# Optimization experiments

Measured on AMD Instinct MI355X. Metric: run time of the kernel, lower is better.

The kernel has to match this reference:

```python
import jax, jax.numpy as jnp
import numpy as np

D_MODEL = 1024
B, S = 4, 4096


def setup_inputs() -> dict:
    key = jax.random.key(0)
    k1, k2, k3, k4, k5 = jax.random.split(key, 5)
    lim = 1.0 / np.sqrt(D_MODEL)  # nn.Linear default init range
    x = jax.random.normal(k1, (B, S, D_MODEL), dtype=jnp.float32)
    mask = jnp.ones((B, S), dtype=jnp.float32)
    W_up = jax.random.uniform(k2, (D_MODEL, D_MODEL), jnp.float32, -lim, lim)
    b_up = jax.random.uniform(k3, (D_MODEL,), jnp.float32, -lim, lim)
    W_f = jax.random.uniform(k4, (D_MODEL, D_MODEL), jnp.float32, -lim, lim)
    b_f = jax.random.uniform(k5, (D_MODEL,), jnp.float32, -lim, lim)
    decay_param = jnp.zeros((1,), dtype=jnp.float32)
    return {"x": x, "mask": mask, "W_up": W_up, "b_up": b_up,
            "W_f": W_f, "b_f": b_f, "decay_param": decay_param}


def _decay_scan(u, decay):
    # h_t = decay * h_{t-1} + u_t  along axis=1, via associative scan.
    # Element: (a, b) representing h -> a*h + b; compose: (a1*a2, b1*a2 + b2).
    a = jnp.broadcast_to(decay, u.shape)

    def combine(c1, c2):
        a1, b1 = c1
        a2, b2 = c2
        return a1 * a2, b1 * a2 + b2

    _, h = jax.lax.associative_scan(combine, (a, u), axis=1)
    return h


def reference(x, mask, W_up, b_up, W_f, b_f, decay_param):
    decay = jax.nn.sigmoid(decay_param)[0]
    # u_i = mask_i * linear_update(x_i)
    u = (jnp.einsum('bsd,ed->bse', x, W_up) + b_up) * mask[..., None]
    # h_t = sum_{i<=t} decay^(t-i) * u_i  (exponential-decay recurrence)
    h = _decay_scan(u, decay)
    return jnp.einsum('bsd,ed->bse', h, W_f) + b_f
```

## Files before the change

### kernel.cpp

```cpp
#include <hip/hip_runtime.h>
#include <hip/hip_bf16.h>
#include <cstdint>
#include <cstddef>

#define DMODEL 1024
#define BATCH  4
#define SEQ    4096
#define BSROWS (BATCH*SEQ)
#define CHUNK  32
#define NCHUNK (SEQ/CHUNK)

typedef __attribute__((ext_vector_type(8))) short bf16x8;
typedef __attribute__((ext_vector_type(4))) float f32x4;


__device__ __forceinline__ unsigned short f2bf(float f) {
  union { float f; uint32_t u; } v; v.f = f;
  uint32_t u = v.u;
  u += 0x7FFFu + ((u >> 16) & 1u);
  return (unsigned short)(u >> 16);
}

__device__ __forceinline__ float sigmoid_dev(const float* dp) {
  return 1.0f / (1.0f + expf(-dp[0]));
}

typedef __attribute__((address_space(1))) void void_g;
typedef __attribute__((address_space(3))) void void_l;

__device__ __forceinline__ void gl2lds16(const void* g, void* l) {
  __builtin_amdgcn_global_load_lds((void_g*)g, (void_l*)l, 16, 0, 0);
}

__global__ __launch_bounds__(256) void prep_kernel(
    const float* __restrict__ x, const float* __restrict__ mask,
    const float* __restrict__ W_up, const float* __restrict__ b_up,
    const float* __restrict__ W_f, const float* __restrict__ dp,
    unsigned short* __restrict__ Wf_bf, unsigned short* __restrict__ WupT,
    float* __restrict__ bb, float* __restrict__ carry,
    float* __restrict__ cbeta) {
  __shared__ float tile[32][33];
  int blk = blockIdx.x;
  int tid = threadIdx.x;

  if (blk < 512) {
    float decay = sigmoid_dev(dp);
    int b = blk / NCHUNK, c = blk % NCHUNK;
    const float4* xp = (const float4*)(x + ((size_t)(b * SEQ + c * CHUNK)) * DMODEL);
    const float* mp = mask + b * SEQ + c * CHUNK;
    float4 h = make_float4(0.f, 0.f, 0.f, 0.f);
    float hb = 0.f;
    #pragma unroll 8
    for (int s = 0; s < CHUNK; ++s) {
      float m = mp[s];
      float4 xv = xp[(size_t)s * (DMODEL / 4) + tid];
      h.x = decay * h.x + m * xv.x;
      h.y = decay * h.y + m * xv.y;
      h.z = decay * h.z + m * xv.z;
      h.w = decay * h.w + m * xv.w;
      hb = decay * hb + m;
    }
    ((float4*)carry)[(size_t)blk * (DMODEL / 4) + tid] = h;
    if (tid == 0) cbeta[blk] = hb;
  } else if (blk < 1536) {
    int i = (blk - 512) * 256 + tid;
    float4 v = ((const float4*)W_f)[i];
    ushort4 o;
    o.x = f2bf(v.x); o.y = f2bf(v.y); o.z = f2bf(v.z); o.w = f2bf(v.w);
    ((ushort4*)Wf_bf)[i] = o;
  } else if (blk < 2560) {
    int id = blk - 1536;
    int bx = id & 31, by = id >> 5;
    int tx = tid & 31, ty = tid >> 5;
    int xx = bx * 32 + tx;
    int y0 = by * 32;
    for (int j = ty; j < 32; j += 8)
      tile[j][tx] = W_up[(size_t)(y0 + j) * DMODEL + xx];
    __syncthreads();
    int ox = by * 32 + tx;
    int oy0 = bx * 32;
    for (int j = ty; j < 32; j += 8)
      WupT[(size_t)(oy0 + j) * DMODEL + ox] = f2bf(tile[tx][j]);
  } else {
    int w = tid >> 6;
    int lane = tid & 63;
    int e = (blk - 2560) * 4 + w;
    float s = 0.f;
    for (int i = lane; i < DMODEL; i += 64)
      s += W_f[(size_t)e * DMODEL + i] * b_up[i];
    #pragma unroll
    for (int off = 32; off; off >>= 1) s += __shfl_down(s, off);
    if (lane == 0) bb[e] = s;
  }
}

__global__ __launch_bounds__(64) void scan_chunk(
    const float* __restrict__ carry, const float* __restrict__ carry_beta,
    const float* __restrict__ dp, float* __restrict__ prefix,
    float* __restrict__ prefix_beta) {
  float decay = sigmoid_dev(dp);
  float dL = powf(decay, (float)CHUNK);
  int gid = blockIdx.x * 64 + threadIdx.x;
  int b = gid >> 10, d = gid & 1023;
  float P = 0.f;
  for (int c = 0; c < NCHUNK; c += 8) {
    float v[8];
    #pragma unroll
    for (int j = 0; j < 8; ++j)
      v[j] = carry[(size_t)(b * NCHUNK + c + j) * DMODEL + d];
    #pragma unroll
    for (int j = 0; j < 8; ++j) {
      prefix[(size_t)(b * NCHUNK + c + j) * DMODEL + d] = P;
      P = dL * P + v[j];
    }
  }
  if (d == 0) {
    float Pb = 0.f;
    for (int c = 0; c < NCHUNK; ++c) {
      prefix_beta[b * NCHUNK + c] = Pb;
      Pb = dL * Pb + carry_beta[b * NCHUNK + c];
    }
  }
}

__global__ __launch_bounds__(256) void mid_kernel(
    const unsigned short* __restrict__ A,
    const unsigned short* __restrict__ Bm,
    unsigned short* __restrict__ Wc,
    const float* __restrict__ x, const float* __restrict__ mask,
    const float* __restrict__ dp,
    const float* __restrict__ prefix, const float* __restrict__ prefix_beta,
    unsigned short* __restrict__ hv, float* __restrict__ hbeta) {
  __shared__ unsigned short As[64 * 32];
  __shared__ unsigned short Bs[64 * 32];
  int tid = threadIdx.x;
  if (blockIdx.x < 256) {
    int vb = blockIdx.x;
    int lane = tid & 63, w = tid >> 6;
    int wm = w & 1, wn = w >> 1;
    int m0 = (vb >> 4) * 64;
    int n0 = (vb & 15) * 64;
    int r = tid >> 2;
    int c8 = (tid & 3) * 8;
    f32x4 acc[2][2] = {};
    for (int k0 = 0; k0 < DMODEL; k0 += 32) {
      gl2lds16(A + (size_t)(m0 + r) * DMODEL + k0 + c8,  As + r * 32 + c8);
      gl2lds16(Bm + (size_t)(n0 + r) * DMODEL + k0 + c8, Bs + r * 32 + c8);
      __syncthreads();
      const bf16x8* Av = (const bf16x8*)As;
      const bf16x8* Bv = (const bf16x8*)Bs;
      int quad = lane >> 4, l16 = lane & 15;
      bf16x8 af[2], bfr[2];
      #pragma unroll
      for (int i = 0; i < 2; i++) {
        af[i]  = Av[(wm * 32 + i * 16 + l16) * 4 + quad];
        bfr[i] = Bv[(wn * 32 + i * 16 + l16) * 4 + quad];
      }
      #pragma unroll
      for (int i = 0; i < 2; i++)
        #pragma unroll
        for (int j = 0; j < 2; j++)
          acc[i][j] = __builtin_amdgcn_mfma_f32_16x16x32_bf16(af[i], bfr[j], acc[i][j], 0, 0, 0);
      __syncthreads();
    }
    int quad = lane >> 4, l16 = lane & 15;
    #pragma unroll
    for (int j = 0; j < 2; j++) {
      int col = n0 + wn * 32 + j * 16 + l16;
      #pragma unroll
      for (int i = 0; i < 2; i++) {
        int rowb = m0 + wm * 32 + i * 16 + quad * 4;
        #pragma unroll
        for (int rr = 0; rr < 4; ++rr)
          Wc[(size_t)(rowb + rr) * DMODEL + col] = f2bf(acc[i][j][rr]);
      }
    }
  } else {
    int vb = blockIdx.x - 256;
    float decay = sigmoid_dev(dp);
    int b = vb / NCHUNK, c = vb % NCHUNK;
    const float4* xp = (const float4*)(x + ((size_t)(b * SEQ + c * CHUNK)) * DMODEL);
    const float* mp = mask + b * SEQ + c * CHUNK;
    float4 h = ((const float4*)prefix)[(size_t)vb * (DMODEL / 4) + tid];
    float hb = prefix_beta[vb];
    #pragma unroll 8
    for (int s = 0; s < CHUNK; ++s) {
      float m = mp[s];
      float4 xv = xp[(size_t)s * (DMODEL / 4) + tid];
      h.x = decay * h.x + m * xv.x;
      h.y = decay * h.y + m * xv.y;
      h.z = decay * h.z + m * xv.z;
      h.w = decay * h.w + m * xv.w;
      hb = decay * hb + m;
      ushort4 o;
      o.x = f2bf(h.x); o.y = f2bf(h.y); o.z = f2bf(h.z); o.w = f2bf(h.w);
      int row = b * SEQ + c * CHUNK + s;
      ((ushort4*)hv)[(size_t)row * (DMODEL / 4) + tid] = o;
      if (tid == 0) hbeta[row] = hb;
    }
  }
}

__global__ __launch_bounds__(256) void gemm_main(
    const unsigned short* __restrict__ A,
    const unsigned short* __restrict__ Bm,
    const float* __restrict__ hbeta,
    const float* __restrict__ bb,
    const float* __restrict__ bias_f,
    float* __restrict__ out) {
  __shared__ unsigned short As[128 * 32];
  __shared__ unsigned short Bs[128 * 32];
  int tid = threadIdx.x;
  int lane = tid & 63, w = tid >> 6;
  int wm = w & 1, wn = w >> 1;
  int m0 = (blockIdx.x & 127) * 128;
  int n0 = (blockIdx.x >> 7) * 128;
  int r = tid >> 2;
  int c8 = (tid & 3) * 8;
  f32x4 acc[4][4] = {};
  for (int k0 = 0; k0 < DMODEL; k0 += 32) {
    gl2lds16(A + (size_t)(m0 + r) * DMODEL + k0 + c8,        As + r * 32 + c8);
    gl2lds16(A + (size_t)(m0 + 64 + r) * DMODEL + k0 + c8,   As + (64 + r) * 32 + c8);
    gl2lds16(Bm + (size_t)(n0 + r) * DMODEL + k0 + c8,       Bs + r * 32 + c8);
    gl2lds16(Bm + (size_t)(n0 + 64 + r) * DMODEL + k0 + c8,  Bs + (64 + r) * 32 + c8);
    __syncthreads();
    const bf16x8* Av = (const bf16x8*)As;
    const bf16x8* Bv = (const bf16x8*)Bs;
    int quad = lane >> 4, l16 = lane & 15;
    bf16x8 af[4], bfr[4];
    #pragma unroll
    for (int i = 0; i < 4; i++) {
      af[i]  = Av[(wm * 64 + i * 16 + l16) * 4 + quad];
      bfr[i] = Bv[(wn * 64 + i * 16 + l16) * 4 + quad];
    }
    #pragma unroll
    for (int i = 0; i < 4; i++)
      #pragma unroll
      for (int j = 0; j < 4; j++)
        acc[i][j] = __builtin_amdgcn_mfma_f32_16x16x32_bf16(af[i], bfr[j], acc[i][j], 0, 0, 0);
    __syncthreads();
  }
  int quad = lane >> 4, l16 = lane & 15;
  #pragma unroll
  for (int j = 0; j < 4; j++) {
    int col = n0 + wn * 64 + j * 16 + l16;
    float bbv = bb[col];
    float bfv = bias_f[col];
    #pragma unroll
    for (int i = 0; i < 4; i++) {
      int rowb = m0 + wm * 64 + i * 16 + quad * 4;
      #pragma unroll
      for (int rr = 0; rr < 4; ++rr) {
        int row = rowb + rr;
        out[(size_t)row * DMODEL + col] = acc[i][j][rr] + hbeta[row] * bbv + bfv;
      }
    }
  }
}


extern "C" void kernel_launch(void* const* d_in, const int* in_sizes, int n_in,
                              void* d_out, int out_size, void* d_ws, size_t ws_size,
                              hipStream_t stream) {
  const float* x    = (const float*)d_in[0];
  const float* mask = (const float*)d_in[1];
  const float* W_up = (const float*)d_in[2];
  const float* b_up = (const float*)d_in[3];
  const float* W_f  = (const float*)d_in[4];
  const float* b_f  = (const float*)d_in[5];
  const float* dp   = (const float*)d_in[6];
  float* out = (float*)d_out;

  char* ws = (char*)d_ws;
  unsigned short* hv    = (unsigned short*)(ws);
  unsigned short* Wc    = (unsigned short*)(ws + 33554432);
  unsigned short* Wf_bf = (unsigned short*)(ws + 35651584);
  unsigned short* WupT  = (unsigned short*)(ws + 37748736);
  float* carry  = (float*)(ws + 39845888);
  float* prefix = (float*)(ws + 41943040);
  float* hbeta  = (float*)(ws + 44040192);
  float* cbeta  = (float*)(ws + 44105728);
  float* pbeta  = (float*)(ws + 44107776);
  float* bb     = (float*)(ws + 44109824);

  prep_kernel<<<2816, 256, 0, stream>>>(x, mask, W_up, b_up, W_f, dp,
                                        Wf_bf, WupT, bb, carry, cbeta);
  scan_chunk<<<64, 64, 0, stream>>>(carry, cbeta, dp, prefix, pbeta);
  mid_kernel<<<768, 256, 0, stream>>>(Wf_bf, WupT, Wc, x, mask, dp,
                                      prefix, pbeta, hv, hbeta);
  gemm_main<<<1024, 256, 0, stream>>>(hv, Wc, hbeta, bb, b_f, out);
}
```

Measured before the change: 203.8 us.

## Decompose scan into local chunk scan plus projected chunk prefix correction

The prep kernel now writes the chunk-local scan of x (in bf16) directly, so the second full pass over x to apply chunk prefixes is gone. Cross-chunk prefixes are instead projected through the combined weight in a small GEMM (pout_kernel) and added in the main GEMM epilogue as decay^(s+1) times the projected prefix. The GEMMs also move to a K-step of 64 with an XOR-swizzled LDS layout to cut bank conflicts. In exchange there is an extra kernel launch and a small GEMM, plus an extra Pout read in the epilogue. Precision changes slightly because local scans are rounded to bf16 separately from the prefix term.

New measurement: 245.6 us. 1.21x slower.

```diff
diff --git a/kernel.cpp b/kernel.cpp
--- a/kernel.cpp
+++ b/kernel.cpp
@@ -9,6 +9,7 @@
 #define BSROWS (BATCH*SEQ)
 #define CHUNK  32
 #define NCHUNK (SEQ/CHUNK)
+#define NCH_T  (BATCH*NCHUNK)
 
 typedef __attribute__((ext_vector_type(8))) short bf16x8;
 typedef __attribute__((ext_vector_type(4))) float f32x4;
@@ -32,12 +33,49 @@
   __builtin_amdgcn_global_load_lds((void_g*)g, (void_l*)l, 16, 0, 0);
 }
 
+__device__ __forceinline__ void kloop64(
+    const unsigned short* __restrict__ A, const unsigned short* __restrict__ B,
+    int m0, int n0, f32x4 acc[2][2],
+    unsigned short* As, unsigned short* Bs, int tid) {
+  int lane = tid & 63, w = tid >> 6, wm = w & 1, wn = w >> 1;
+  int quad = lane >> 4, l16 = lane & 15;
+  int r = tid >> 3, cch = tid & 7;
+  int g = cch ^ (r & 7);
+  const bf16x8* Av = (const bf16x8*)As;
+  const bf16x8* Bv = (const bf16x8*)Bs;
+  for (int k0 = 0; k0 < DMODEL; k0 += 64) {
+    gl2lds16(A + (size_t)(m0 + r) * DMODEL + k0 + g * 8,      As + r * 64 + cch * 8);
+    gl2lds16(A + (size_t)(m0 + 32 + r) * DMODEL + k0 + g * 8, As + (32 + r) * 64 + cch * 8);
+    gl2lds16(B + (size_t)(n0 + r) * DMODEL + k0 + g * 8,      Bs + r * 64 + cch * 8);
+    gl2lds16(B + (size_t)(n0 + 32 + r) * DMODEL + k0 + g * 8, Bs + (32 + r) * 64 + cch * 8);
+    __syncthreads();
+    #pragma unroll
+    for (int kk = 0; kk < 2; ++kk) {
+      bf16x8 af[2], bfr[2];
+      #pragma unroll
+      for (int i = 0; i < 2; ++i) {
+        int rowA = wm * 32 + i * 16 + l16;
+        af[i]  = Av[rowA * 8 + ((kk * 4 + quad) ^ (l16 & 7))];
+        int rowB = wn * 32 + i * 16 + l16;
+        bfr[i] = Bv[rowB * 8 + ((kk * 4 + quad) ^ (l16 & 7))];
+      }
+      #pragma unroll
+      for (int i = 0; i < 2; ++i)
+        #pragma unroll
+        for (int j = 0; j < 2; ++j)
+          acc[i][j] = __builtin_amdgcn_mfma_f32_16x16x32_bf16(af[i], bfr[j], acc[i][j], 0, 0, 0);
+    }
+    __syncthreads();
+  }
+}
+
 __global__ __launch_bounds__(256) void prep_kernel(
     const float* __restrict__ x, const float* __restrict__ mask,
     const float* __restrict__ W_up, const float* __restrict__ b_up,
     const float* __restrict__ W_f, const float* __restrict__ dp,
     unsigned short* __restrict__ Wf_bf, unsigned short* __restrict__ WupT,
-    float* __restrict__ bb, float* __restrict__ carry,
+    float* __restrict__ bb, unsigned short* __restrict__ hv,
+    float* __restrict__ carry, float* __restrict__ lbeta,
     float* __restrict__ cbeta) {
   __shared__ float tile[32][33];
   int blk = blockIdx.x;
@@ -46,8 +84,9 @@
   if (blk < 512) {
     float decay = sigmoid_dev(dp);
     int b = blk / NCHUNK, c = blk % NCHUNK;
-    const float4* xp = (const float4*)(x + ((size_t)(b * SEQ + c * CHUNK)) * DMODEL);
-    const float* mp = mask + b * SEQ + c * CHUNK;
+    int base = b * SEQ + c * CHUNK;
+    const float4* xp = (const float4*)(x + (size_t)base * DMODEL);
+    const float* mp = mask + base;
     float4 h = make_float4(0.f, 0.f, 0.f, 0.f);
     float hb = 0.f;
     #pragma unroll 8
@@ -59,6 +98,10 @@
       h.z = decay * h.z + m * xv.z;
       h.w = decay * h.w + m * xv.w;
       hb = decay * hb + m;
+      ushort4 o;
+      o.x = f2bf(h.x); o.y = f2bf(h.y); o.z = f2bf(h.z); o.w = f2bf(h.w);
+      ((ushort4*)hv)[(size_t)(base + s) * (DMODEL / 4) + tid] = o;
+      if (tid == 0) lbeta[base + s] = hb;
     }
     ((float4*)carry)[(size_t)blk * (DMODEL / 4) + tid] = h;
     if (tid == 0) cbeta[blk] = hb;
@@ -94,109 +137,91 @@
   }
 }
 
-__global__ __launch_bounds__(64) void scan_chunk(
-    const float* __restrict__ carry, const float* __restrict__ carry_beta,
-    const float* __restrict__ dp, float* __restrict__ prefix,
-    float* __restrict__ prefix_beta) {
-  float decay = sigmoid_dev(dp);
-  float dL = powf(decay, (float)CHUNK);
-  int gid = blockIdx.x * 64 + threadIdx.x;
-  int b = gid >> 10, d = gid & 1023;
-  float P = 0.f;
-  for (int c = 0; c < NCHUNK; c += 8) {
-    float v[8];
-    #pragma unroll
-    for (int j = 0; j < 8; ++j)
-      v[j] = carry[(size_t)(b * NCHUNK + c + j) * DMODEL + d];
-    #pragma unroll
-    for (int j = 0; j < 8; ++j) {
-      prefix[(size_t)(b * NCHUNK + c + j) * DMODEL + d] = P;
-      P = dL * P + v[j];
-    }
-  }
-  if (d == 0) {
-    float Pb = 0.f;
-    for (int c = 0; c < NCHUNK; ++c) {
-      prefix_beta[b * NCHUNK + c] = Pb;
-      Pb = dL * Pb + carry_beta[b * NCHUNK + c];
-    }
-  }
-}
-
-__global__ __launch_bounds__(256) void mid_kernel(
-    const unsigned short* __restrict__ A,
-    const unsigned short* __restrict__ Bm,
+__global__ __launch_bounds__(256) void mid2_kernel(
+    const unsigned short* __restrict__ Wf_bf,
+    const unsigned short* __restrict__ WupT,
     unsigned short* __restrict__ Wc,
-    const float* __restrict__ x, const float* __restrict__ mask,
+    const float* __restrict__ carry, const float* __restrict__ cbeta,
     const float* __restrict__ dp,
-    const float* __restrict__ prefix, const float* __restrict__ prefix_beta,
-    unsigned short* __restrict__ hv, float* __restrict__ hbeta) {
-  __shared__ unsigned short As[64 * 32];
-  __shared__ unsigned short Bs[64 * 32];
+    unsigned short* __restrict__ Pbf, float* __restrict__ pbeta) {
+  __shared__ unsigned short As[64 * 64];
+  __shared__ unsigned short Bs[64 * 64];
   int tid = threadIdx.x;
   if (blockIdx.x < 256) {
-    int vb = blockIdx.x;
-    int lane = tid & 63, w = tid >> 6;
-    int wm = w & 1, wn = w >> 1;
-    int m0 = (vb >> 4) * 64;
-    int n0 = (vb & 15) * 64;
-    int r = tid >> 2;
-    int c8 = (tid & 3) * 8;
+    int mt = blockIdx.x >> 4, nt = blockIdx.x & 15;
     f32x4 acc[2][2] = {};
-    for (int k0 = 0; k0 < DMODEL; k0 += 32) {
-      gl2lds16(A + (size_t)(m0 + r) * DMODEL + k0 + c8,  As + r * 32 + c8);
-      gl2lds16(Bm + (size_t)(n0 + r) * DMODEL + k0 + c8, Bs + r * 32 + c8);
-      __syncthreads();
-      const bf16x8* Av = (const bf16x8*)As;
-      const bf16x8* Bv = (const bf16x8*)Bs;
-      int quad = lane >> 4, l16 = lane & 15;
-      bf16x8 af[2], bfr[2];
-      #pragma unroll
-      for (int i = 0; i < 2; i++) {
-        af[i]  = Av[(wm * 32 + i * 16 + l16) * 4 + quad];
-        bfr[i] = Bv[(wn * 32 + i * 16 + l16) * 4 + quad];
-      }
-      #pragma unroll
-      for (int i = 0; i < 2; i++)
-        #pragma unroll
-        for (int j = 0; j < 2; j++)
-          acc[i][j] = __builtin_amdgcn_mfma_f32_16x16x32_bf16(af[i], bfr[j], acc[i][j], 0, 0, 0);
-      __syncthreads();
-    }
+    kloop64(Wf_bf, WupT, mt * 64, nt * 64, acc, As, Bs, tid);
+    int lane = tid & 63, w = tid >> 6, wm = w & 1, wn = w >> 1;
     int quad = lane >> 4, l16 = lane & 15;
     #pragma unroll
-    for (int j = 0; j < 2; j++) {
-      int col = n0 + wn * 32 + j * 16 + l16;
-      #pragma unroll
-      for (int i = 0; i < 2; i++) {
-        int rowb = m0 + wm * 32 + i * 16 + quad * 4;
+    for (int j = 0; j < 2; ++j) {
+      int col = nt * 64 + wn * 32 + j * 16 + l16;
+      #pragma unroll
+      for (int i = 0; i < 2; ++i) {
+        int rowb = mt * 64 + wm * 32 + i * 16 + quad * 4;
         #pragma unroll
         for (int rr = 0; rr < 4; ++rr)
           Wc[(size_t)(rowb + rr) * DMODEL + col] = f2bf(acc[i][j][rr]);
       }
     }
   } else {
-    int vb = blockIdx.x - 256;
     float decay = sigmoid_dev(dp);
-    int b = vb / NCHUNK, c = vb % NCHUNK;
-    const float4* xp = (const float4*)(x + ((size_t)(b * SEQ + c * CHUNK)) * DMODEL);
-    const float* mp = mask + b * SEQ + c * CHUNK;
-    float4 h = ((const float4*)prefix)[(size_t)vb * (DMODEL / 4) + tid];
-    float hb = prefix_beta[vb];
-    #pragma unroll 8
-    for (int s = 0; s < CHUNK; ++s) {
-      float m = mp[s];
-      float4 xv = xp[(size_t)s * (DMODEL / 4) + tid];
-      h.x = decay * h.x + m * xv.x;
-      h.y = decay * h.y + m * xv.y;
-      h.z = decay * h.z + m * xv.z;
-      h.w = decay * h.w + m * xv.w;
-      hb = decay * hb + m;
-      ushort4 o;
-      o.x = f2bf(h.x); o.y = f2bf(h.y); o.z = f2bf(h.z); o.w = f2bf(h.w);
-      int row = b * SEQ + c * CHUNK + s;
-      ((ushort4*)hv)[(size_t)row * (DMODEL / 4) + tid] = o;
-      if (tid == 0) hbeta[row] = hb;
+    float dL = powf(decay, (float)CHUNK);
+    int gid = (blockIdx.x - 256) * 256 + tid;
+    int b = gid >> 10, dd = gid & 1023;
+    float P = 0.f;
+    for (int c0 = 0; c0 < NCHUNK; c0 += 8) {
+      float v[8];
+      #pragma unroll
+      for (int j = 0; j < 8; ++j)
+        v[j] = carry[(size_t)(b * NCHUNK + c0 + j) * DMODEL + dd];
+      #pragma unroll
+      for (int j = 0; j < 8; ++j) {
+        Pbf[(size_t)(b * NCHUNK + c0 + j) * DMODEL + dd] = f2bf(P);
+        P = dL * P + v[j];
+      }
+    }
+    if (dd == 0) {
+      float Pb = 0.f;
+      for (int c0 = 0; c0 < NCHUNK; c0 += 16) {
+        float v[16];
+        #pragma unroll
+        for (int j = 0; j < 16; ++j) v[j] = cbeta[b * NCHUNK + c0 + j];
+        #pragma unroll
+        for (int j = 0; j < 16; ++j) {
+          pbeta[b * NCHUNK + c0 + j] = Pb;
+          Pb = dL * Pb + v[j];
+        }
+      }
+    }
+  }
+}
+
+__global__ __launch_bounds__(256) void pout_kernel(
+    const unsigned short* __restrict__ Pbf,
+    const unsigned short* __restrict__ Wc,
+    const float* __restrict__ pbeta, const float* __restrict__ bb,
+    float* __restrict__ Pout) {
+  __shared__ unsigned short As[64 * 64];
+  __shared__ unsigned short Bs[64 * 64];
+  int tid = threadIdx.x;
+  int mt = blockIdx.x >> 4, nt = blockIdx.x & 15;
+  f32x4 acc[2][2] = {};
+  kloop64(Pbf, Wc, mt * 64, nt * 64, acc, As, Bs, tid);
+  int lane = tid & 63, w = tid >> 6, wm = w & 1, wn = w >> 1;
+  int quad = lane >> 4, l16 = lane & 15;
+  #pragma unroll
+  for (int j = 0; j < 2; ++j) {
+    int col = nt * 64 + wn * 32 + j * 16 + l16;
+    float bbv = bb[col];
+    #pragma unroll
+    for (int i = 0; i < 2; ++i) {
+      int rowb = mt * 64 + wm * 32 + i * 16 + quad * 4;
+      #pragma unroll
+      for (int rr = 0; rr < 4; ++rr) {
+        int row = rowb + rr;
+        Pout[(size_t)row * DMODEL + col] = acc[i][j][rr] + pbeta[row] * bbv;
+      }
     }
   }
 }
@@ -204,55 +229,70 @@
 __global__ __launch_bounds__(256) void gemm_main(
     const unsigned short* __restrict__ A,
     const unsigned short* __restrict__ Bm,
-    const float* __restrict__ hbeta,
+    const float* __restrict__ Pout,
+    const float* __restrict__ lbeta,
     const float* __restrict__ bb,
     const float* __restrict__ bias_f,
+    const float* __restrict__ dp,
     float* __restrict__ out) {
-  __shared__ unsigned short As[128 * 32];
-  __shared__ unsigned short Bs[128 * 32];
+  __shared__ unsigned short As[128 * 64];
+  __shared__ unsigned short Bs[128 * 64];
+  __shared__ float dpow[CHUNK];
   int tid = threadIdx.x;
-  int lane = tid & 63, w = tid >> 6;
-  int wm = w & 1, wn = w >> 1;
+  if (tid < CHUNK) {
+    float decay = sigmoid_dev(dp);
+    dpow[tid] = powf(decay, (float)(tid + 1));
+  }
+  int lane = tid & 63, w = tid >> 6, wm = w & 1, wn = w >> 1;
+  int quad = lane >> 4, l16 = lane & 15;
+  int r = tid >> 3, cch = tid & 7;
+  int g = cch ^ (r & 7);
   int m0 = (blockIdx.x & 127) * 128;
   int n0 = (blockIdx.x >> 7) * 128;
-  int r = tid >> 2;
-  int c8 = (tid & 3) * 8;
   f32x4 acc[4][4] = {};
-  for (int k0 = 0; k0 < DMODEL; k0 += 32) {
-    gl2lds16(A + (size_t)(m0 + r) * DMODEL + k0 + c8,        As + r * 32 + c8);
-    gl2lds16(A + (size_t)(m0 + 64 + r) * DMODEL + k0 + c8,   As + (64 + r) * 32 + c8);
-    gl2lds16(Bm + (size_t)(n0 + r) * DMODEL + k0 + c8,       Bs + r * 32 + c8);
-    gl2lds16(Bm + (size_t)(n0 + 64 + r) * DMODEL + k0 + c8,  Bs + (64 + r) * 32 + c8);
-    __syncthreads();
-    const bf16x8* Av = (const bf16x8*)As;
-    const bf16x8* Bv = (const bf16x8*)Bs;
-    int quad = lane >> 4, l16 = lane & 15;
-    bf16x8 af[4], bfr[4];
-    #pragma unroll
-    for (int i = 0; i < 4; i++) {
-      af[i]  = Av[(wm * 64 + i * 16 + l16) * 4 + quad];
-      bfr[i] = Bv[(wn * 64 + i * 16 + l16) * 4 + quad];
-    }
-    #pragma unroll
-    for (int i = 0; i < 4; i++)
-      #pragma unroll
-      for (int j = 0; j < 4; j++)
-        acc[i][j] = __builtin_amdgcn_mfma_f32_16x16x32_bf16(af[i], bfr[j], acc[i][j], 0, 0, 0);
-    __syncthreads();
-  }
-  int quad = lane >> 4, l16 = lane & 15;
+  const bf16x8* Av = (const bf16x8*)As;
+  const bf16x8* Bv = (const bf16x8*)Bs;
+  for (int k0 = 0; k0 < DMODEL; k0 += 64) {
+    #pragma unroll
+    for (int q = 0; q < 4; ++q) {
+      gl2lds16(A  + (size_t)(m0 + q * 32 + r) * DMODEL + k0 + g * 8,
+               As + (q * 32 + r) * 64 + cch * 8);
+      gl2lds16(Bm + (size_t)(n0 + q * 32 + r) * DMODEL + k0 + g * 8,
+               Bs + (q * 32 + r) * 64 + cch * 8);
+    }
+    __syncthreads();
+    #pragma unroll
+    for (int kk = 0; kk < 2; ++kk) {
+      bf16x8 af[4], bfr[4];
+      #pragma unroll
+      for (int i = 0; i < 4; ++i) {
+        int rowA = wm * 64 + i * 16 + l16;
+        af[i]  = Av[rowA * 8 + ((kk * 4 + quad) ^ (l16 & 7))];
+        int rowB = wn * 64 + i * 16 + l16;
+        bfr[i] = Bv[rowB * 8 + ((kk * 4 + quad) ^ (l16 & 7))];
+      }
+      #pragma unroll
+      for (int i = 0; i < 4; ++i)
+        #pragma unroll
+        for (int j = 0; j < 4; ++j)
+          acc[i][j] = __builtin_amdgcn_mfma_f32_16x16x32_bf16(af[i], bfr[j], acc[i][j], 0, 0, 0);
+    }
+    __syncthreads();
+  }
   #pragma unroll
-  for (int j = 0; j < 4; j++) {
+  for (int j = 0; j < 4; ++j) {
     int col = n0 + wn * 64 + j * 16 + l16;
     float bbv = bb[col];
     float bfv = bias_f[col];
     #pragma unroll
-    for (int i = 0; i < 4; i++) {
+    for (int i = 0; i < 4; ++i) {
       int rowb = m0 + wm * 64 + i * 16 + quad * 4;
       #pragma unroll
       for (int rr = 0; rr < 4; ++rr) {
         int row = rowb + rr;
-        out[(size_t)row * DMODEL + col] = acc[i][j][rr] + hbeta[row] * bbv + bfv;
+        float po = Pout[(size_t)(row >> 5) * DMODEL + col];
+        out[(size_t)row * DMODEL + col] =
+            acc[i][j][rr] + dpow[row & 31] * po + lbeta[row] * bbv + bfv;
       }
     }
   }
@@ -277,16 +317,17 @@
   unsigned short* Wf_bf = (unsigned short*)(ws + 35651584);
   unsigned short* WupT  = (unsigned short*)(ws + 37748736);
   float* carry  = (float*)(ws + 39845888);
-  float* prefix = (float*)(ws + 41943040);
-  float* hbeta  = (float*)(ws + 44040192);
-  float* cbeta  = (float*)(ws + 44105728);
-  float* pbeta  = (float*)(ws + 44107776);
-  float* bb     = (float*)(ws + 44109824);
+  unsigned short* Pbf = (unsigned short*)(ws + 41943040);
+  float* Pout   = (float*)(ws + 42991616);
+  float* lbeta  = (float*)(ws + 45088768);
+  float* cbeta  = (float*)(ws + 45154304);
+  float* pbeta  = (float*)(ws + 45156352);
+  float* bb     = (float*)(ws + 45158400);
 
   prep_kernel<<<2816, 256, 0, stream>>>(x, mask, W_up, b_up, W_f, dp,
-                                        Wf_bf, WupT, bb, carry, cbeta);
-  scan_chunk<<<64, 64, 0, stream>>>(carry, cbeta, dp, prefix, pbeta);
-  mid_kernel<<<768, 256, 0, stream>>>(Wf_bf, WupT, Wc, x, mask, dp,
-                                      prefix, pbeta, hv, hbeta);
-  gemm_main<<<1024, 256, 0, stream>>>(hv, Wc, hbeta, bb, b_f, out);
-}
+                                        Wf_bf, WupT, bb, hv, carry, lbeta, cbeta);
+  mid2_kernel<<<272, 256, 0, stream>>>(Wf_bf, WupT, Wc, carry, cbeta, dp,
+                                       Pbf, pbeta);
+  pout_kernel<<<128, 256, 0, stream>>>(Pbf, Wc, pbeta, bb, Pout);
+  gemm_main<<<1024, 256, 0, stream>>>(hv, Wc, Pout, lbeta, bb, b_f, dp, out);
+}
```
